# Kernel optimization log

Hardware: AMD Instinct MI355X
Metric: run time of the kernel (lower is better)

## Reference

```python
import jax, jax.numpy as jnp
import numpy as np

B, S, E, H, L = 4, 1024, 1024, 16, 4
D = E // H
MAX_POS = 1024
NI, NS = 10000, 1000
W_SCALE = 0.02


def setup_inputs() -> dict:
    key = jax.random.key(0)
    ks = jax.random.split(key, 24)
    r = lambda k, sh: jax.random.normal(k, sh, dtype=jnp.float32) * W_SCALE
    return {
        'item_inputs': jax.random.randint(ks[0], (B, S), 0, NI),
        'skill_inputs': jax.random.randint(ks[1], (B, S), 0, NS),
        'label_inputs': jax.random.randint(ks[2], (B, S), 0, 2),
        'item_ids': jax.random.randint(ks[3], (B, S), 0, NI),
        'skill_ids': jax.random.randint(ks[4], (B, S), 0, NS),
        'emb_item': r(ks[5], (NI, E)),
        'emb_skill': r(ks[6], (NS, E)),
        'W_in': r(ks[7], (E, 2 * E)),
        'b_in': r(ks[8], (E,)),
        'Wq': r(ks[9], (L, E, E)),
        'bq': r(ks[10], (L, E)),
        'Wk': r(ks[11], (L, E, E)),
        'bk': r(ks[12], (L, E)),
        'Wv': r(ks[13], (L, E, E)),
        'bv': r(ks[14], (L, E)),
        'Wg': r(ks[15], (L, H, E)),
        'bg': r(ks[16], (L, H)),
        'pos_key': r(ks[17], (L, MAX_POS, D)),
        'Wl': r(ks[18], (L, 3, E, E)),
        'bl': r(ks[19], (L, 3, E)),
        'W_out': r(ks[20], (1, E)),
        'b_out': r(ks[21], (1,)),
    }


def _forward(item_inputs, skill_inputs, emb_item, emb_skill, W_in, b_in,
             Wq, bq, Wk, bk, Wv, bv, Wg, bg, pos_key, Wl, bl, W_out, b_out):
    # input embedding: concat(item, skill) -> linear
    x = jnp.concatenate([emb_item[item_inputs], emb_skill[skill_inputs]], axis=-1)
    x = x @ W_in.T + b_in  # [B, S, E]
    pos_ids = jnp.clip(jnp.arange(S), 0, MAX_POS - 1)
    inv_sqrt_d = 1.0 / np.sqrt(D).astype(np.float32)
    for l in range(L):
        # NOTE (faithful to source): k and v are computed from q0 = linear_q(x)
        q0 = x @ Wq[l].T + bq[l]
        k = q0 @ Wk[l].T + bk[l]
        v = q0 @ Wv[l].T + bv[l]
        # global bias: [B, S, H] -> [B, H, S, 1] (broadcast over key dim)
        glo = jnp.transpose(k @ Wg[l].T + bg[l], (0, 2, 1))[..., None]
        qh = q0.reshape(B, S, H, D).transpose(0, 2, 1, 3)  # [B,H,S,D]
        kh = k.reshape(B, S, H, D).transpose(0, 2, 1, 3)
        vh = v.reshape(B, S, H, D).transpose(0, 2, 1, 3)
        pe = pos_key[l][pos_ids]  # [S, D]
        scores = (jnp.einsum('bhqd,bhkd->bhqk', qh, kh)
                  + glo
                  + jnp.einsum('bhqd,kd->bhqk', qh, pe)) * inv_sqrt_d
        prob = jax.nn.softmax(scores, axis=-1)
        o = jnp.einsum('bhqk,bhkd->bhqd', prob, vh)
        o = o.transpose(0, 2, 1, 3).reshape(B, S, E)
        for i in range(3):  # GELU MLP stack
            o = jax.nn.gelu(o @ Wl[l, i].T + bl[l, i], approximate=False)
        x = o
    out = x @ W_out.T + b_out  # [B, S, 1]
    return out[..., 0]


def reference(item_inputs, skill_inputs, label_inputs, item_ids, skill_ids,
              emb_item, emb_skill, W_in, b_in, Wq, bq, Wk, bk, Wv, bv,
              Wg, bg, pos_key, Wl, bl, W_out, b_out):
    return _forward(item_inputs, skill_inputs, emb_item, emb_skill, W_in, b_in,
                    Wq, bq, Wk, bk, Wv, bv, Wg, bg, pos_key, Wl, bl, W_out, b_out)
```

## Files before the change

kernel.cpp:

```cpp
#include <hip/hip_runtime.h>
#include <hip/hip_bf16.h>


#define B_ 4
#define S_ 1024
#define E_ 1024
#define H_ 16
#define D_ 64
#define L_ 4
#define M_ (B_ * S_)
#define EE (E_ * E_)

typedef __attribute__((ext_vector_type(8))) __bf16 bf16x8;
typedef __attribute__((ext_vector_type(4))) __bf16 bf16x4;
typedef __attribute__((ext_vector_type(4))) float f32x4;
typedef __attribute__((ext_vector_type(8))) unsigned short u16x8;

__device__ __forceinline__ float bf2f(unsigned short u) {
    union { unsigned int i; float f; } x;
    x.i = ((unsigned int)u) << 16;
    return x.f;
}
__device__ __forceinline__ float gelu_exact(float x) {
    return 0.5f * x * (1.0f + erff(x * 0.70710678118654752f));
}

__device__ __forceinline__ size_t kpack_idx(int m, int col) {
    const int b = m >> 10, srow = m & (S_ - 1);
    const int h = col >> 6, d = col & 63;
    const int bh = b * H_ + h;
    const int kt = srow >> 6, kb = (srow >> 4) & 3, l15 = srow & 15;
    const int kc = d >> 5, lhi = (d >> 3) & 3, j = d & 7;
    const int frag = ((bh * 16 + kt) * 4 + kb) * 2 + kc;
    return (size_t)frag * 512 + (size_t)(lhi * 16 + l15) * 8 + j;
}
__device__ __forceinline__ size_t vpack_idx(int m, int col) {
    const int b = m >> 10, key = m & (S_ - 1);
    const int h = col >> 6, d = col & 63;
    const int bh = b * H_ + h;
    const int kt = key >> 6;
    const int k6 = key & 63;
    const int kc = k6 >> 5, kl = k6 & 31;
    const int lhi = (kl >> 2) & 3;
    const int j = ((kl >> 4) << 2) | (kl & 3);
    const int db = d >> 4, l15 = d & 15;
    const int frag = ((bh * 16 + kt) * 4 + db) * 2 + kc;
    return (size_t)frag * 512 + (size_t)(lhi * 16 + l15) * 8 + j;
}

__global__ __launch_bounds__(256) void cvt_f32_bf16(
    const float* __restrict__ in, __bf16* __restrict__ out, int n) {
    const int i = (blockIdx.x * 256 + threadIdx.x) * 4;
    if (i >= n) return;
    const float4 v = *(const float4*)(in + i);
    __bf16* o = out + i;
    o[0] = (__bf16)v.x; o[1] = (__bf16)v.y; o[2] = (__bf16)v.z; o[3] = (__bf16)v.w;
}

__global__ __launch_bounds__(256) void cvt_all_weights(
    const float* __restrict__ Wq, const float* __restrict__ Wk,
    const float* __restrict__ Wv, const float* __restrict__ Wl,
    __bf16* __restrict__ out) {
    const int i = (blockIdx.x * 256 + threadIdx.x) * 4;
    const int l = i / (6 * EE);
    const int r = i - l * 6 * EE;
    const int mat = r >> 20;
    const int off = r & (EE - 1);
    const float* src = (mat == 0) ? Wq + (size_t)l * EE
                     : (mat == 1) ? Wk + (size_t)l * EE
                     : (mat == 2) ? Wv + (size_t)l * EE
                                  : Wl + ((size_t)l * 3 + (mat - 3)) * EE;
    const float4 v = *(const float4*)(src + off);
    __bf16* o = out + i;
    o[0] = (__bf16)v.x; o[1] = (__bf16)v.y; o[2] = (__bf16)v.z; o[3] = (__bf16)v.w;
}

__global__ __launch_bounds__(256) void embed_gather(
    const int* __restrict__ item_idx, const int* __restrict__ skill_idx,
    const float* __restrict__ emb_item, const float* __restrict__ emb_skill,
    __bf16* __restrict__ Xc) {
    const int r = blockIdx.x;
    const int c = threadIdx.x * 8;
    const float* s = (c < E_) ? emb_item + (size_t)item_idx[r] * E_ + c
                              : emb_skill + (size_t)skill_idx[r] * E_ + (c - E_);
    const float4 a = *(const float4*)s;
    const float4 b = *(const float4*)(s + 4);
    __bf16* o = Xc + (size_t)r * 2048 + c;
    o[0] = (__bf16)a.x; o[1] = (__bf16)a.y; o[2] = (__bf16)a.z; o[3] = (__bf16)a.w;
    o[4] = (__bf16)b.x; o[5] = (__bf16)b.y; o[6] = (__bf16)b.z; o[7] = (__bf16)b.w;
}

template <int ACT, int ADD_PE, int PACK>
__global__ __launch_bounds__(256) void gemm_bf16(
    const __bf16* __restrict__ A, const __bf16* __restrict__ Bm,
    const float* __restrict__ bias, __bf16* __restrict__ C, int K,
    const float* __restrict__ pe, const float* __restrict__ bias2) {
    __shared__ __bf16 As[2][128 * 64];
    __shared__ __bf16 Bs[2][64 * 64];
    const int tid = threadIdx.x;
    const int lane = tid & 63;
    const int wid = tid >> 6;
    const int wm = wid >> 1;
    const int wn = wid & 1;
    const int l15 = lane & 15, lhi = lane >> 4;

    const int gx = gridDim.x;
    const int id = blockIdx.y * gx + blockIdx.x;
    const int nwg = gx * gridDim.y;
    const int swz = (id & 7) * (nwg >> 3) + (id >> 3);
    const int m0 = (swz / gx) * 128;
    const int n0 = (swz % gx) * 64;

    const __bf16* pa[4];
    int laoff[4];
#pragma unroll
    for (int j = 0; j < 4; ++j) {
        const int ca = wid * 256 + j * 64 + lane;
        const int row = ca >> 3, ch = ca & 7;
        pa[j] = A + (size_t)(m0 + row) * K + ((ch ^ (row & 7)) << 3);
        laoff[j] = ca * 8;
    }
    const __bf16* pb[2];
    int lboff[2];
#pragma unroll
    for (int j = 0; j < 2; ++j) {
        const int cb = wid * 128 + j * 64 + lane;
        const int row = cb >> 3, ch = cb & 7;
        pb[j] = Bm + (size_t)(n0 + row) * K + ((ch ^ (row & 7)) << 3);
        lboff[j] = cb * 8;
    }

    int aoff[4][2], boff[2][2];
#pragma unroll
    for (int mi = 0; mi < 4; ++mi) {
        const int row = wm * 64 + mi * 16 + l15;
#pragma unroll
        for (int kc = 0; kc < 2; ++kc)
            aoff[mi][kc] = row * 64 + (((kc * 4 + lhi) ^ (row & 7)) << 3);
    }
#pragma unroll
    for (int ni = 0; ni < 2; ++ni) {
        const int row = wn * 32 + ni * 16 + l15;
#pragma unroll
        for (int kc = 0; kc < 2; ++kc)
            boff[ni][kc] = row * 64 + (((kc * 4 + lhi) ^ (row & 7)) << 3);
    }

    f32x4 acc[4][2] = {};
    const int NT = K >> 6;

#pragma unroll
    for (int j = 0; j < 4; ++j)
        __builtin_amdgcn_global_load_lds(
            (const __attribute__((address_space(1))) unsigned int*)(pa[j]),
            (__attribute__((address_space(3))) unsigned int*)(&As[0][0] + laoff[j]),
            16, 0, 0);
#pragma unroll
    for (int j = 0; j < 2; ++j)
        __builtin_amdgcn_global_load_lds(
            (const __attribute__((address_space(1))) unsigned int*)(pb[j]),
            (__attribute__((address_space(3))) unsigned int*)(&Bs[0][0] + lboff[j]),
            16, 0, 0);

    for (int t = 0; t < NT; ++t) {
        const int cur = t & 1;
        __syncthreads();
        if (t + 1 < NT) {
            const size_t koff = (size_t)(t + 1) << 6;
#pragma unroll
            for (int j = 0; j < 4; ++j)
                __builtin_amdgcn_global_load_lds(
                    (const __attribute__((address_space(1))) unsigned int*)(pa[j] + koff),
                    (__attribute__((address_space(3))) unsigned int*)(
                        &As[cur ^ 1][0] + laoff[j]), 16, 0, 0);
#pragma unroll
            for (int j = 0; j < 2; ++j)
                __builtin_amdgcn_global_load_lds(
                    (const __attribute__((address_space(1))) unsigned int*)(pb[j] + koff),
                    (__attribute__((address_space(3))) unsigned int*)(
                        &Bs[cur ^ 1][0] + lboff[j]), 16, 0, 0);
        }
        bf16x8 af[4][2], bfr[2][2];
#pragma unroll
        for (int mi = 0; mi < 4; ++mi)
#pragma unroll
            for (int kc = 0; kc < 2; ++kc)
                af[mi][kc] = *(const bf16x8*)(&As[cur][0] + aoff[mi][kc]);
#pragma unroll
        for (int ni = 0; ni < 2; ++ni)
#pragma unroll
            for (int kc = 0; kc < 2; ++kc)
                bfr[ni][kc] = *(const bf16x8*)(&Bs[cur][0] + boff[ni][kc]);
#pragma unroll
        for (int mi = 0; mi < 4; ++mi)
#pragma unroll
            for (int ni = 0; ni < 2; ++ni)
#pragma unroll
                for (int kc = 0; kc < 2; ++kc)
                    acc[mi][ni] = __builtin_amdgcn_mfma_f32_16x16x32_bf16(
                        af[mi][kc], bfr[ni][kc], acc[mi][ni], 0, 0, 0);
    }

    const int ccol0 = n0 + wn * 32 + l15;
    const int crow0 = m0 + wm * 64 + (lhi << 2);
#pragma unroll
    for (int mi = 0; mi < 4; ++mi) {
#pragma unroll
        for (int ni = 0; ni < 2; ++ni) {
            const int col = ccol0 + ni * 16;
            float bsum;
            if (PACK == 3) bsum = (col < 1024) ? bias[col] : bias2[col - 1024];
            else bsum = bias[col];
#pragma unroll
            for (int r = 0; r < 4; ++r) {
                const int row = crow0 + mi * 16 + r;
                float v = acc[mi][ni][r] + bsum;
                if (ADD_PE) v += pe[((row & (S_ - 1)) << 6) + (col & (D_ - 1))];
                if (ACT) v = gelu_exact(v);
                if (PACK == 0) {
                    C[(size_t)row * E_ + col] = (__bf16)v;
                } else if (PACK == 1) {
                    C[kpack_idx(row, col)] = (__bf16)v;
                } else if (PACK == 2) {
                    C[vpack_idx(row, col)] = (__bf16)v;
                } else {
                    if (col < 1024) {
                        v += pe[((row & (S_ - 1)) << 6) + (col & (D_ - 1))];
                        C[kpack_idx(row, col)] = (__bf16)v;
                    } else {
                        C[(size_t)M_ * E_ + vpack_idx(row, col - 1024)] = (__bf16)v;
                    }
                }
            }
        }
    }
}

__global__ __launch_bounds__(512) void attn_mfma(
    const __bf16* __restrict__ Q, const __bf16* __restrict__ Kp,
    const __bf16* __restrict__ Vp, __bf16* __restrict__ O) {
    __shared__ __bf16 Slds[2][2][8 * 512];
    const int tid = threadIdx.x;
    const int lane = tid & 63;
    const int w = tid >> 6;
    const int l15 = lane & 15, lhi = lane >> 4;

    const int id = blockIdx.y * gridDim.x + blockIdx.x;
    const int swz = (id & 7) * 64 + (id >> 3);
    const int q0 = (swz & 7) * 128 + w * 16;
    const int bh = swz >> 3;
    const int bb = bh >> 4, hh = bh & 15;

    bf16x8 qf[2];
    {
        const __bf16* qrow =
            Q + (size_t)(bb * S_ + q0 + l15) * E_ + hh * 64 + lhi * 8;
#pragma unroll
        for (int kc = 0; kc < 2; ++kc) {
            const u16x8 raw = *(const u16x8*)(qrow + kc * 32);
            bf16x8 v;
#pragma unroll
            for (int j = 0; j < 8; ++j) v[j] = (__bf16)(bf2f(raw[j]) * 0.125f);
            qf[kc] = v;
        }
    }

    const __bf16* kpw = Kp + ((size_t)bh * 16 * 8 + w) * 512 + lane * 8;
    const __bf16* vpw = Vp + ((size_t)bh * 16 * 8 + w) * 512 + lane * 8;

    float m_l = -1e30f, l_l = 0.f;
    f32x4 oacc[4] = {};

    __builtin_amdgcn_global_load_lds(
        (const __attribute__((address_space(1))) unsigned int*)(kpw),
        (__attribute__((address_space(3))) unsigned int*)(&Slds[0][0][w * 512]),
        16, 0, 0);
    __builtin_amdgcn_global_load_lds(
        (const __attribute__((address_space(1))) unsigned int*)(vpw),
        (__attribute__((address_space(3))) unsigned int*)(&Slds[0][1][w * 512]),
        16, 0, 0);

#pragma unroll 2
    for (int kt = 0; kt < S_ / 64; ++kt) {
        const int cur = kt & 1;
        __syncthreads();
        if (kt < S_ / 64 - 1) {
            const size_t fo = (size_t)(kt + 1) * 8 * 512;
            __builtin_amdgcn_global_load_lds(
                (const __attribute__((address_space(1))) unsigned int*)(kpw + fo),
                (__attribute__((address_space(3))) unsigned int*)(
                    &Slds[cur ^ 1][0][w * 512]), 16, 0, 0);
            __builtin_amdgcn_global_load_lds(
                (const __attribute__((address_space(1))) unsigned int*)(vpw + fo),
                (__attribute__((address_space(3))) unsigned int*)(
                    &Slds[cur ^ 1][1][w * 512]), 16, 0, 0);
        }
        const __bf16* kl = &Slds[cur][0][0];
        const __bf16* vl = &Slds[cur][1][0];
        f32x4 s[4];
#pragma unroll
        for (int kb = 0; kb < 4; ++kb) {
            const bf16x8 k0 = *(const bf16x8*)(kl + (kb * 2 + 0) * 512 + lane * 8);
            const bf16x8 k1 = *(const bf16x8*)(kl + (kb * 2 + 1) * 512 + lane * 8);
            f32x4 z = {};
            z = __builtin_amdgcn_mfma_f32_16x16x32_bf16(k0, qf[0], z, 0, 0, 0);
            s[kb] = __builtin_amdgcn_mfma_f32_16x16x32_bf16(k1, qf[1], z, 0, 0, 0);
        }
        float mx0 = fmaxf(fmaxf(s[0][0], s[0][1]), fmaxf(s[0][2], s[0][3]));
        float mx1 = fmaxf(fmaxf(s[1][0], s[1][1]), fmaxf(s[1][2], s[1][3]));
        float mx2 = fmaxf(fmaxf(s[2][0], s[2][1]), fmaxf(s[2][2], s[2][3]));
        float mx3 = fmaxf(fmaxf(s[3][0], s[3][1]), fmaxf(s[3][2], s[3][3]));
        float mx = fmaxf(fmaxf(mx0, mx1), fmaxf(mx2, mx3));
        mx = fmaxf(mx, __shfl_xor(mx, 16));
        mx = fmaxf(mx, __shfl_xor(mx, 32));
        const float mnew = fmaxf(m_l, mx);
        const float corr = __expf(m_l - mnew);
        float p[4][4];
        float rs = 0.f;
#pragma unroll
        for (int kb = 0; kb < 4; ++kb) {
            float sb = 0.f;
#pragma unroll
            for (int r = 0; r < 4; ++r) {
                p[kb][r] = __expf(s[kb][r] - mnew);
                sb += p[kb][r];
            }
            rs += sb;
        }
        rs += __shfl_xor(rs, 16);
        rs += __shfl_xor(rs, 32);
        l_l = l_l * corr + rs;
        m_l = mnew;
#pragma unroll
        for (int db = 0; db < 4; ++db)
#pragma unroll
            for (int r = 0; r < 4; ++r) oacc[db][r] *= corr;
        bf16x8 pf[2];
#pragma unroll
        for (int kc = 0; kc < 2; ++kc) {
            bf16x8 v;
#pragma unroll
            for (int r = 0; r < 4; ++r) {
                v[r] = (__bf16)p[kc * 2][r];
                v[r + 4] = (__bf16)p[kc * 2 + 1][r];
            }
            pf[kc] = v;
        }
#pragma unroll
        for (int db = 0; db < 4; ++db) {
            const bf16x8 v0 = *(const bf16x8*)(vl + (db * 2 + 0) * 512 + lane * 8);
            const bf16x8 v1 = *(const bf16x8*)(vl + (db * 2 + 1) * 512 + lane * 8);
            oacc[db] = __builtin_amdgcn_mfma_f32_16x16x32_bf16(v0, pf[0], oacc[db], 0, 0, 0);
            oacc[db] = __builtin_amdgcn_mfma_f32_16x16x32_bf16(v1, pf[1], oacc[db], 0, 0, 0);
        }
    }
    const float inv_l = 1.f / l_l;
    __bf16* orow = O + (size_t)(bb * S_ + q0 + l15) * E_ + hh * 64 + lhi * 4;
#pragma unroll
    for (int db = 0; db < 4; ++db) {
        bf16x4 ov;
#pragma unroll
        for (int r = 0; r < 4; ++r) ov[r] = (__bf16)(oacc[db][r] * inv_l);
        *(bf16x4*)(orow + db * 16) = ov;
    }
}

__global__ __launch_bounds__(256) void final_proj(
    const __bf16* __restrict__ X, const float* __restrict__ Wout,
    const float* __restrict__ bout, float* __restrict__ out) {
    const int wid = threadIdx.x >> 6, lane = threadIdx.x & 63;
    const int m = blockIdx.x * 4 + wid;
    const __bf16* xrow = X + (size_t)m * E_;
    float acc = 0.f;
#pragma unroll
    for (int c = 0; c < 2; ++c) {
        const int idx = c * 512 + lane * 8;
        const u16x8 xv = *(const u16x8*)(xrow + idx);
        const float4 w1 = *(const float4*)(Wout + idx);
        const float4 w2 = *(const float4*)(Wout + idx + 4);
        acc += bf2f(xv[0]) * w1.x + bf2f(xv[1]) * w1.y + bf2f(xv[2]) * w1.z +
               bf2f(xv[3]) * w1.w + bf2f(xv[4]) * w2.x + bf2f(xv[5]) * w2.y +
               bf2f(xv[6]) * w2.z + bf2f(xv[7]) * w2.w;
    }
#pragma unroll
    for (int off = 32; off; off >>= 1) acc += __shfl_xor(acc, off, 64);
    if (lane == 0) out[m] = acc + bout[0];
}

extern "C" void kernel_launch(void* const* d_in, const int* in_sizes, int n_in,
                              void* d_out, int out_size, void* d_ws, size_t ws_size,
                              hipStream_t stream) {
    const int* item_inputs = (const int*)d_in[0];
    const int* skill_inputs = (const int*)d_in[1];
    const float* emb_item = (const float*)d_in[5];
    const float* emb_skill = (const float*)d_in[6];
    const float* W_in = (const float*)d_in[7];
    const float* b_in = (const float*)d_in[8];
    const float* Wq = (const float*)d_in[9];
    const float* bq = (const float*)d_in[10];
    const float* Wk = (const float*)d_in[11];
    const float* bk = (const float*)d_in[12];
    const float* Wv = (const float*)d_in[13];
    const float* bv = (const float*)d_in[14];
    const float* pos_key = (const float*)d_in[17];
    const float* Wl = (const float*)d_in[18];
    const float* bl = (const float*)d_in[19];
    const float* W_out = (const float*)d_in[20];
    const float* b_out = (const float*)d_in[21];
    float* out = (float*)d_out;

    const size_t SZ = (size_t)M_ * E_;
    __bf16* Xc = (__bf16*)d_ws;
    __bf16* X = Xc + (size_t)M_ * 2048;
    __bf16* Qb = X + SZ;
    __bf16* Kp = Qb + SZ;
    __bf16* Vp = Kp + SZ;
    __bf16* Winb = Vp + SZ;
    __bf16* Wall = Winb + 2 * EE;

    const dim3 gg(E_ / 64, M_ / 128);
    const dim3 ggkv(2 * E_ / 64, M_ / 128);
    const dim3 bb(256);

    embed_gather<<<dim3(M_), bb, 0, stream>>>(item_inputs, skill_inputs,
                                              emb_item, emb_skill, Xc);
    cvt_f32_bf16<<<dim3(2 * EE / 1024), bb, 0, stream>>>(W_in, Winb, 2 * EE);
    cvt_all_weights<<<dim3(L_ * 6 * EE / 1024), bb, 0, stream>>>(Wq, Wk, Wv, Wl, Wall);
    gemm_bf16<0, 0, 0><<<gg, bb, 0, stream>>>(Xc, Winb, b_in, X, 2048, nullptr, nullptr);

    for (int l = 0; l < L_; ++l) {
        __bf16* Wbuf = Wall + (size_t)l * 6 * EE;
        const float* pe_l = pos_key + (size_t)l * S_ * D_;
        gemm_bf16<0, 0, 0><<<gg, bb, 0, stream>>>(X, Wbuf + 0 * EE, bq + l * E_, Qb, E_, nullptr, nullptr);
        gemm_bf16<0, 0, 3><<<ggkv, bb, 0, stream>>>(Qb, Wbuf + 1 * EE, bk + l * E_, Kp, E_, pe_l, bv + l * E_);
        attn_mfma<<<dim3(S_ / 128, B_ * H_), dim3(512), 0, stream>>>(Qb, Kp, Vp, X);
        gemm_bf16<1, 0, 0><<<gg, bb, 0, stream>>>(X, Wbuf + 3 * EE, bl + (l * 3 + 0) * E_, Qb, E_, nullptr, nullptr);
        gemm_bf16<1, 0, 0><<<gg, bb, 0, stream>>>(Qb, Wbuf + 4 * EE, bl + (l * 3 + 1) * E_, Kp, E_, nullptr, nullptr);
        gemm_bf16<1, 0, 0><<<gg, bb, 0, stream>>>(Kp, Wbuf + 5 * EE, bl + (l * 3 + 2) * E_, X, E_, nullptr, nullptr);
    }
    final_proj<<<dim3(M_ / 4), bb, 0, stream>>>(X, W_out, b_out, out);
}
```

Baseline: 596.4 us.

## Triple-buffer GEMM LDS tiles with explicit vmcnt waits and MFMA priority

Moves the bf16 GEMM main loop from double to triple buffering of the A/B LDS tiles, so two tiles are in flight while one is being consumed. It uses hand-placed s_waitcnt vmcnt counts and raw s_barrier in place of __syncthreads, and issues the next prefetch only after fragments are in registers. MFMA sections are wrapped in s_setprio to favour math issue. The change raises LDS use to 72KB per block, which may reduce occupancy, and the hard-coded vmcnt values depend on the exact count of six loads per stage.

```diff
diff --git a/kernel.cpp b/kernel.cpp
--- a/kernel.cpp
+++ b/kernel.cpp
@@ -95,8 +95,8 @@
     const __bf16* __restrict__ A, const __bf16* __restrict__ Bm,
     const float* __restrict__ bias, __bf16* __restrict__ C, int K,
     const float* __restrict__ pe, const float* __restrict__ bias2) {
-    __shared__ __bf16 As[2][128 * 64];
-    __shared__ __bf16 Bs[2][64 * 64];
+    __shared__ __bf16 As[3][128 * 64];
+    __shared__ __bf16 Bs[3][64 * 64];
     const int tid = threadIdx.x;
     const int lane = tid & 63;
     const int wid = tid >> 6;
@@ -149,48 +149,55 @@
     f32x4 acc[4][2] = {};
     const int NT = K >> 6;
 
-#pragma unroll
-    for (int j = 0; j < 4; ++j)
-        __builtin_amdgcn_global_load_lds(
-            (const __attribute__((address_space(1))) unsigned int*)(pa[j]),
-            (__attribute__((address_space(3))) unsigned int*)(&As[0][0] + laoff[j]),
-            16, 0, 0);
-#pragma unroll
-    for (int j = 0; j < 2; ++j)
-        __builtin_amdgcn_global_load_lds(
-            (const __attribute__((address_space(1))) unsigned int*)(pb[j]),
-            (__attribute__((address_space(3))) unsigned int*)(&Bs[0][0] + lboff[j]),
-            16, 0, 0);
-
+    auto STAGE = [&](int tt, int buf) {
+        const size_t koff = (size_t)tt << 6;
+#pragma unroll
+        for (int j = 0; j < 4; ++j)
+            __builtin_amdgcn_global_load_lds(
+                (const __attribute__((address_space(1))) unsigned int*)(pa[j] + koff),
+                (__attribute__((address_space(3))) unsigned int*)(
+                    &As[buf][0] + laoff[j]), 16, 0, 0);
+#pragma unroll
+        for (int j = 0; j < 2; ++j)
+            __builtin_amdgcn_global_load_lds(
+                (const __attribute__((address_space(1))) unsigned int*)(pb[j] + koff),
+                (__attribute__((address_space(3))) unsigned int*)(
+                    &Bs[buf][0] + lboff[j]), 16, 0, 0);
+    };
+
+    STAGE(0, 0);
+    STAGE(1, 1);
+    STAGE(2, 2);
+
+    int cur = 0;
     for (int t = 0; t < NT; ++t) {
-        const int cur = t & 1;
-        __syncthreads();
-        if (t + 1 < NT) {
-            const size_t koff = (size_t)(t + 1) << 6;
-#pragma unroll
-            for (int j = 0; j < 4; ++j)
-                __builtin_amdgcn_global_load_lds(
-                    (const __attribute__((address_space(1))) unsigned int*)(pa[j] + koff),
-                    (__attribute__((address_space(3))) unsigned int*)(
-                        &As[cur ^ 1][0] + laoff[j]), 16, 0, 0);
-#pragma unroll
-            for (int j = 0; j < 2; ++j)
-                __builtin_amdgcn_global_load_lds(
-                    (const __attribute__((address_space(1))) unsigned int*)(pb[j] + koff),
-                    (__attribute__((address_space(3))) unsigned int*)(
-                        &Bs[cur ^ 1][0] + lboff[j]), 16, 0, 0);
-        }
+        if (t < NT - 2)
+            asm volatile("s_waitcnt vmcnt(12)" ::: "memory");
+        else if (t == NT - 2)
+            asm volatile("s_waitcnt vmcnt(6)" ::: "memory");
+        else
+            asm volatile("s_waitcnt vmcnt(0)" ::: "memory");
+        __builtin_amdgcn_s_barrier();
+
+        const __bf16* Ab = &As[cur][0];
+        const __bf16* Bb = &Bs[cur][0];
         bf16x8 af[4][2], bfr[2][2];
 #pragma unroll
         for (int mi = 0; mi < 4; ++mi)
 #pragma unroll
             for (int kc = 0; kc < 2; ++kc)
-                af[mi][kc] = *(const bf16x8*)(&As[cur][0] + aoff[mi][kc]);
+                af[mi][kc] = *(const bf16x8*)(Ab + aoff[mi][kc]);
 #pragma unroll
         for (int ni = 0; ni < 2; ++ni)
 #pragma unroll
             for (int kc = 0; kc < 2; ++kc)
-                bfr[ni][kc] = *(const bf16x8*)(&Bs[cur][0] + boff[ni][kc]);
+                bfr[ni][kc] = *(const bf16x8*)(Bb + boff[ni][kc]);
+        asm volatile("s_waitcnt lgkmcnt(0)" ::: "memory");
+        __builtin_amdgcn_s_barrier();
+
+        if (t + 3 < NT) STAGE(t + 3, cur);
+
+        __builtin_amdgcn_s_setprio(1);
 #pragma unroll
         for (int mi = 0; mi < 4; ++mi)
 #pragma unroll
@@ -199,6 +206,8 @@
                 for (int kc = 0; kc < 2; ++kc)
                     acc[mi][ni] = __builtin_amdgcn_mfma_f32_16x16x32_bf16(
                         af[mi][kc], bfr[ni][kc], acc[mi][ni], 0, 0, 0);
+        __builtin_amdgcn_s_setprio(0);
+        cur = (cur == 2) ? 0 : cur + 1;
     }
 
     const int ccol0 = n0 + wn * 32 + l15;
```

After: 586.0 us. Within noise of the previous version (-1.7%).
